# Performance work log

Measured on AMD Instinct MI355X. Metric: run time of the kernel, lower is better.

The kernel has to match this reference:

```python
import jax, jax.numpy as jnp
import numpy as np

NUM_CODES = 1024
CODE_DIM = 64
EMA_DECAY = 0.99
COMMIT_W = 0.25
EPS = 1e-5
B = 262144


def setup_inputs() -> dict:
    key = jax.random.key(0)
    k1, k2, k3, k4 = jax.random.split(key, 4)
    z = jax.random.normal(k1, (B, CODE_DIM), dtype=jnp.float32)
    weight = jax.random.normal(k2, (NUM_CODES, CODE_DIM), dtype=jnp.float32)
    ema_cluster_size = jax.random.uniform(k3, (NUM_CODES,), dtype=jnp.float32)
    ema_embed_sum = jax.random.normal(k4, (NUM_CODES, CODE_DIM), dtype=jnp.float32)
    return {"z": z, "weight": weight, "ema_cluster_size": ema_cluster_size,
            "ema_embed_sum": ema_embed_sum}


def reference(z, weight, ema_cluster_size, ema_embed_sum):
    # Squared Euclidean distances (argmin equivalent to cdist argmin)
    # d2[b,k] = ||z_b||^2 - 2 z_b . w_k + ||w_k||^2
    z2 = jnp.sum(z * z, axis=-1, keepdims=True)          # (B, 1)
    w2 = jnp.sum(weight * weight, axis=-1)               # (K,)
    d2 = z2 - 2.0 * (z @ weight.T) + w2[None, :]         # (B, K)
    indices = jnp.argmin(d2, axis=-1)                    # (B,)
    z_q = weight[indices]                                # gather with OLD weights

    # EMA codebook update (training, ema_update=True)
    ones = jnp.ones((z.shape[0],), dtype=z.dtype)
    cluster_size = jax.ops.segment_sum(ones, indices, num_segments=NUM_CODES)
    embed_sum = jax.ops.segment_sum(z, indices, num_segments=NUM_CODES)
    new_cs = EMA_DECAY * ema_cluster_size + (1.0 - EMA_DECAY) * cluster_size
    new_es = EMA_DECAY * ema_embed_sum + (1.0 - EMA_DECAY) * embed_sum
    n = jnp.sum(new_cs)
    smoothed = (new_cs + EPS) / (n + NUM_CODES * EPS) * n
    new_weight = new_es / smoothed[:, None]

    # commitment loss (z detached in torch; pure value here)
    vq_loss = COMMIT_W * jnp.mean((z - z_q) ** 2)

    # straight-through estimator
    z_q_st = z + jax.lax.stop_gradient(z_q - z)
    return z_q_st, indices, vq_loss, new_cs, new_es, new_weight
```

## Files before the change

### kernel.cpp

```cpp
#include <hip/hip_runtime.h>

typedef __attribute__((ext_vector_type(8))) short bf16x8;
typedef __attribute__((ext_vector_type(4))) float f32x4;

#define B_ROWS 262144
#define K_CODES 1024
#define DIM 64
#define SDELTA 0.015f

#define OUT_ZQ 0
#define OUT_IDX 16777216
#define OUT_LOSS 17039360
#define OUT_NEWCS 17039361
#define OUT_NEWES 17040385
#define OUT_NEWW 17105921

#define WS_LOSS   0
#define WS_QCOUNT 1
#define WS_W2     16
#define WS_SMOOTH 1040
#define WS_WHIP   2064
#define WS_WLOP   34832
#define WS_CPART  67600
#define WS_EPART  100368
#define WS_MINI   2197520
#define WS_QUEUE  2459664

static __device__ __forceinline__ unsigned short f2bf(float x) {
    unsigned u = __float_as_uint(x);
    return (unsigned short)((u + 0x7fffu + ((u >> 16) & 1u)) >> 16);
}
static __device__ __forceinline__ float bf2f(unsigned short u) {
    return __uint_as_float(((unsigned)u) << 16);
}

static __device__ __forceinline__ float red16(float x) {
    int v;
    v = __builtin_amdgcn_update_dpp(0, __float_as_int(x), 0x128, 0xF, 0xF, true);
    x += __int_as_float(v);
    v = __builtin_amdgcn_update_dpp(0, __float_as_int(x), 0x124, 0xF, 0xF, true);
    x += __int_as_float(v);
    v = __builtin_amdgcn_update_dpp(0, __float_as_int(x), 0x122, 0xF, 0xF, true);
    x += __int_as_float(v);
    v = __builtin_amdgcn_update_dpp(0, __float_as_int(x), 0x121, 0xF, 0xF, true);
    x += __int_as_float(v);
    return x;
}

static __device__ __forceinline__ void cvt_frag(const float* zrow, bf16x8& hi, bf16x8& lo) {
    float4 f0 = *(const float4*)zrow;
    float4 f1 = *(const float4*)(zrow + 4);
    float tf[8] = {f0.x, f0.y, f0.z, f0.w, f1.x, f1.y, f1.z, f1.w};
#pragma unroll
    for (int j = 0; j < 8; ++j) {
        unsigned short h = f2bf(tf[j]);
        hi[j] = (short)h;
        lo[j] = (short)f2bf(tf[j] - bf2f(h));
    }
}

__global__ __launch_bounds__(256) void vq_prep(const float* __restrict__ w,
                                               float* __restrict__ ws) {
    int b = blockIdx.x, tid = threadIdx.x;
    if (b < 4) {
        int k = b * 256 + tid;
        const float4* w4 = (const float4*)(w + (size_t)k * DIM);
        float s = 0.f;
#pragma unroll
        for (int j = 0; j < 16; ++j) {
            float4 v = w4[j];
            s += v.x * v.x + v.y * v.y + v.z * v.z + v.w * v.w;
        }
        ws[WS_W2 + k] = s;
    } else {
        int i = (b - 4) * 256 + tid;
        int p = i & 1023, c = i >> 10;
        int code = c * 128 + ((p >> 7) << 4) + (p & 15);
        int octet = ((p >> 6) & 1) * 4 + ((p >> 4) & 3);
        const float* src = w + (size_t)code * DIM + octet * 8;
        float4 f0 = *(const float4*)src;
        float4 f1 = *(const float4*)(src + 4);
        float tf[8] = {f0.x, f0.y, f0.z, f0.w, f1.x, f1.y, f1.z, f1.w};
        bf16x8 hv, lv;
#pragma unroll
        for (int j = 0; j < 8; ++j) {
            unsigned short hb = f2bf(tf[j]);
            hv[j] = (short)hb;
            lv[j] = (short)f2bf(tf[j] - bf2f(hb));
        }
        ((bf16x8*)(ws + WS_WHIP))[i] = hv;
        ((bf16x8*)(ws + WS_WLOP))[i] = lv;
    }
}

__global__ __launch_bounds__(256)
__attribute__((amdgpu_waves_per_eu(3, 4))) void vq_screen_kernel(
    const float* __restrict__ z, float* __restrict__ ws) {
    __shared__ float lds_w2h[K_CODES];

    int tid = threadIdx.x;
    int l = tid & 63, wave = tid >> 6;
    int m = l & 15, q = l >> 4;

    {
        float4 wv = ((const float4*)(ws + WS_W2))[tid];
        float4 hv;
        hv.x = -0.5f * wv.x;
        hv.y = -0.5f * wv.y;
        hv.z = -0.5f * wv.z;
        hv.w = -0.5f * wv.w;
        *(float4*)&lds_w2h[tid * 4] = hv;
    }

    int rowbase = blockIdx.x * 256 + wave * 64;
    bf16x8 zhi[4][2], zlo[4][2];
#pragma unroll
    for (int g = 0; g < 4; ++g) {
        const float* zr = z + (size_t)(rowbase + g * 16 + m) * DIM + q * 8;
        cvt_frag(zr, zhi[g][0], zlo[g][0]);
        cvt_frag(zr + 32, zhi[g][1], zlo[g][1]);
    }

    float kv[4], k2[4];
#pragma unroll
    for (int g = 0; g < 4; ++g) { kv[g] = -3.4e38f; k2[g] = -3.4e38f; }

    const bf16x8* __restrict__ gh = (const bf16x8*)(ws + WS_WHIP);
    const bf16x8* __restrict__ gl = (const bf16x8*)(ws + WS_WLOP);

    __syncthreads();

    for (int cch = 0; cch < 8; ++cch) {
#pragma unroll 2
        for (int tg = 0; tg < 8; ++tg) {
            int gi = cch * 1024 + tg * 128 + l;
            bf16x8 bh0 = gh[gi];
            bf16x8 bh1 = gh[gi + 64];
            bf16x8 bl0 = gl[gi];
            bf16x8 bl1 = gl[gi + 64];
            unsigned cbase = (unsigned)(cch * 128 + tg * 16 + q * 4);
            unsigned ibase = (unsigned)((cch * 8 + tg) * 4);
            f32x4 cinit = *(const f32x4*)&lds_w2h[cbase];
#pragma unroll
            for (int g = 0; g < 4; ++g) {
                f32x4 acc = cinit;
                acc = __builtin_amdgcn_mfma_f32_16x16x32_bf16(bh0, zlo[g][0], acc, 0, 0, 0);
                acc = __builtin_amdgcn_mfma_f32_16x16x32_bf16(bl0, zhi[g][0], acc, 0, 0, 0);
                acc = __builtin_amdgcn_mfma_f32_16x16x32_bf16(bh1, zlo[g][1], acc, 0, 0, 0);
                acc = __builtin_amdgcn_mfma_f32_16x16x32_bf16(bl1, zhi[g][1], acc, 0, 0, 0);
                acc = __builtin_amdgcn_mfma_f32_16x16x32_bf16(bh0, zhi[g][0], acc, 0, 0, 0);
                acc = __builtin_amdgcn_mfma_f32_16x16x32_bf16(bh1, zhi[g][1], acc, 0, 0, 0);
                float a0 = __uint_as_float((__float_as_uint(acc[0]) & 0xFFFFFF00u) | ibase);
                float a1 = __uint_as_float((__float_as_uint(acc[1]) & 0xFFFFFF00u) | (ibase + 1u));
                float a2 = __uint_as_float((__float_as_uint(acc[2]) & 0xFFFFFF00u) | (ibase + 2u));
                float a3 = __uint_as_float((__float_as_uint(acc[3]) & 0xFFFFFF00u) | (ibase + 3u));
                float m01 = fmaxf(a0, a1), n01 = fminf(a0, a1);
                float m23 = fmaxf(a2, a3), n23 = fminf(a2, a3);
                float top = fmaxf(m01, m23);
                float sec = fmaxf(fmaxf(fminf(m01, m23), n01), n23);
                k2[g] = fmaxf(fmaxf(k2[g], sec), fminf(kv[g], top));
                kv[g] = fmaxf(kv[g], top);
            }
        }
    }

    float mv[4], m2[4];
    int mi[4];
#pragma unroll
    for (int g = 0; g < 4; ++g) {
        unsigned kb = __float_as_uint(kv[g]);
        unsigned i8 = kb & 255u;
        mi[g] = (int)((i8 >> 5) * 128 + ((i8 >> 2) & 7) * 16 + (unsigned)q * 4 + (i8 & 3));
        mv[g] = __uint_as_float(kb & 0xFFFFFF00u);
        m2[g] = __uint_as_float(__float_as_uint(k2[g]) & 0xFFFFFF00u);
    }
#pragma unroll
    for (int o = 16; o < 64; o <<= 1) {
#pragma unroll
        for (int g = 0; g < 4; ++g) {
            float ov = __shfl_xor(mv[g], o, 64);
            float ov2 = __shfl_xor(m2[g], o, 64);
            int oi = __shfl_xor(mi[g], o, 64);
            float nm2 = fmaxf(fmaxf(m2[g], ov2), fminf(mv[g], ov));
            bool take = (ov > mv[g]) || (ov == mv[g] && oi < mi[g]);
            mv[g] = take ? ov : mv[g];
            mi[g] = take ? oi : mi[g];
            m2[g] = nm2;
        }
    }
    if (q == 0) {
#pragma unroll
        for (int g = 0; g < 4; ++g) {
            bool amb = (mv[g] - m2[g]) <= SDELTA;
            ((int*)ws)[WS_MINI + rowbase + g * 16 + m] = mi[g] | (amb ? 0x80000000 : 0);
        }
    }
}

__global__ __launch_bounds__(256) void vq_gather_kernel(
    const float* __restrict__ z, const float* __restrict__ w,
    float* __restrict__ ws, float* __restrict__ out) {
    __shared__ float lred[4];
    int tid = threadIdx.x;
    int lane = tid & 63, wave = tid >> 6;
    int rsub = lane >> 4;
    int d4 = lane & 15;
    int wavebase = blockIdx.x * 256 + wave * 64;

    int encv[16];
#pragma unroll
    for (int s = 0; s < 16; ++s)
        encv[s] = ((const int*)ws)[WS_MINI + wavebase + s * 4 + rsub];

    float lsum = 0.f;
#pragma unroll
    for (int s = 0; s < 16; ++s) {
        int row = wavebase + s * 4 + rsub;
        int enc = encv[s];
        if (enc >= 0) {
            float4 x = ((const float4*)(z + (size_t)row * DIM))[d4];
            float4 qv = ((const float4*)(w + (size_t)enc * DIM))[d4];
            float4 st;
            st.x = x.x + (qv.x - x.x);
            st.y = x.y + (qv.y - x.y);
            st.z = x.z + (qv.z - x.z);
            st.w = x.w + (qv.w - x.w);
            ((float4*)(out + OUT_ZQ + (size_t)row * DIM))[d4] = st;
            float e0 = x.x - qv.x, e1 = x.y - qv.y, e2 = x.z - qv.z, e3 = x.w - qv.w;
            lsum += e0 * e0;
            lsum += e1 * e1;
            lsum += e2 * e2;
            lsum += e3 * e3;
            if (d4 == 0) out[OUT_IDX + row] = (float)enc;
        } else if (d4 == 0) {
            int pos = atomicAdd((int*)ws + WS_QCOUNT, 1);
            ((int*)ws)[WS_QUEUE + pos] = row;
        }
    }
#pragma unroll
    for (int o = 32; o; o >>= 1) lsum += __shfl_down(lsum, o, 64);
    if (lane == 0) lred[wave] = lsum;
    __syncthreads();
    if (tid == 0) atomicAdd(ws + WS_LOSS, lred[0] + lred[1] + lred[2] + lred[3]);
}

__global__ __launch_bounds__(256) void vq_fixup_kernel(
    const float* __restrict__ z, const float* __restrict__ w,
    float* __restrict__ ws, float* __restrict__ out) {
    const float* __restrict__ w2 = ws + WS_W2;
    __shared__ float sdd[4][4];
    __shared__ int sbi[4][4];
    int count = ((const int*)ws)[WS_QCOUNT];
    int tid = threadIdx.x;
    int lane = tid & 63, wave = tid >> 6;
    int sub = lane >> 4, d4 = lane & 15;
    float lacc = 0.f;
    for (int q0 = blockIdx.x * 4; q0 < count; q0 += gridDim.x * 4) {
        int qi = q0 + sub;
        bool active = qi < count;
        int row = ((const int*)ws)[WS_QUEUE + (active ? qi : 0)];
        float4 zx = ((const float4*)(z + (size_t)row * DIM))[d4];
        float zp = zx.x * zx.x;
        zp = fmaf(zx.y, zx.y, zp);
        zp = fmaf(zx.z, zx.z, zp);
        zp = fmaf(zx.w, zx.w, zp);
        float z2 = red16(zp);
        float best = 3.4e38f;
        int bi = 0;
        int c0 = wave * 256;
#pragma unroll 4
        for (int cc = 0; cc < 256; ++cc) {
            int c = c0 + cc;
            float4 wv4 = ((const float4*)(w + (size_t)c * DIM))[d4];
            float p = zx.x * wv4.x;
            p = fmaf(zx.y, wv4.y, p);
            p = fmaf(zx.z, wv4.z, p);
            p = fmaf(zx.w, wv4.w, p);
            p = red16(p);
            float dd = (z2 - 2.f * p) + w2[c];
            if (dd < best) { best = dd; bi = c; }
        }
        if (d4 == 0) { sdd[wave][sub] = best; sbi[wave][sub] = bi; }
        __syncthreads();
        if (wave == 0 && active) {
            float fb = sdd[0][sub];
            int fbi = sbi[0][sub];
#pragma unroll
            for (int v = 1; v < 4; ++v) {
                float od = sdd[v][sub];
                int oi = sbi[v][sub];
                if (od < fb || (od == fb && oi < fbi)) { fb = od; fbi = oi; }
            }
            float4 qv = ((const float4*)(w + (size_t)fbi * DIM))[d4];
            float4 st;
            st.x = zx.x + (qv.x - zx.x);
            st.y = zx.y + (qv.y - zx.y);
            st.z = zx.z + (qv.z - zx.z);
            st.w = zx.w + (qv.w - zx.w);
            ((float4*)(out + OUT_ZQ + (size_t)row * DIM))[d4] = st;
            float e0 = zx.x - qv.x, e1 = zx.y - qv.y;
            float e2 = zx.z - qv.z, e3 = zx.w - qv.w;
            float ls = e0 * e0 + e1 * e1 + e2 * e2 + e3 * e3;
            ls = red16(ls);
            if (d4 == 0) {
                out[OUT_IDX + row] = (float)fbi;
                lacc += ls;
            }
        }
        __syncthreads();
    }
    lacc += __shfl_xor(lacc, 16, 64);
    lacc += __shfl_xor(lacc, 32, 64);
    if (tid == 0 && lacc != 0.f) atomicAdd(ws + WS_LOSS, lacc);
}

__global__ __launch_bounds__(1024) void vq_embed_kernel(
    const float* __restrict__ z, const float* __restrict__ idx_f,
    float* __restrict__ ws) {
    __shared__ float eacc[128 * DIM];
    __shared__ float ecnt[128];
    __shared__ int lists[16][256];
    int b = blockIdx.x;
    int cs = b & 7, rs = b >> 3;
    float lo = (float)(cs * 128), hi = lo + 128.f;
    int tid = threadIdx.x;
    int wave = tid >> 6, lane = tid & 63;

#pragma unroll
    for (int j = 0; j < 8; ++j) eacc[j * 1024 + tid] = 0.f;
    if (tid < 128) ecnt[tid] = 0.f;
    __syncthreads();

    const float4* idx4 = (const float4*)idx_f;
    unsigned long long lanebits = (1ull << lane) - 1ull;
    for (int it = 0; it < 2; ++it) {
        int base = rs * 8192 + wave * 512 + it * 256;
        float4 f = idx4[(base >> 2) + lane];
        int cnt = 0;
#pragma unroll
        for (int c = 0; c < 4; ++c) {
            float fv = (c == 0) ? f.x : (c == 1) ? f.y : (c == 2) ? f.z : f.w;
            bool match = (fv >= lo && fv < hi);
            unsigned long long mmask = __ballot(match);
            if (match) {
                int pos = cnt + __popcll(mmask & lanebits);
                int row = base + 4 * lane + c;
                int local = (int)fv - cs * 128;
                lists[wave][pos] = (row << 7) | local;
                atomicAdd(&ecnt[local], 1.f);
            }
            cnt += __popcll(mmask);
        }
        int j = 0;
        for (; j + 4 <= cnt; j += 4) {
            int e0 = lists[wave][j], e1 = lists[wave][j + 1];
            int e2 = lists[wave][j + 2], e3 = lists[wave][j + 3];
            float v0 = z[(size_t)(e0 >> 7) * DIM + lane];
            float v1 = z[(size_t)(e1 >> 7) * DIM + lane];
            float v2 = z[(size_t)(e2 >> 7) * DIM + lane];
            float v3 = z[(size_t)(e3 >> 7) * DIM + lane];
            atomicAdd(&eacc[(e0 & 127) * DIM + lane], v0);
            atomicAdd(&eacc[(e1 & 127) * DIM + lane], v1);
            atomicAdd(&eacc[(e2 & 127) * DIM + lane], v2);
            atomicAdd(&eacc[(e3 & 127) * DIM + lane], v3);
        }
        for (; j < cnt; ++j) {
            int e = lists[wave][j];
            float v = z[(size_t)(e >> 7) * DIM + lane];
            atomicAdd(&eacc[(e & 127) * DIM + lane], v);
        }
    }
    __syncthreads();
#pragma unroll
    for (int j = 0; j < 8; ++j)
        ws[WS_EPART + (size_t)b * 8192 + j * 1024 + tid] = eacc[j * 1024 + tid];
    if (tid < 128) ws[WS_CPART + b * 128 + tid] = ecnt[tid];
}

__global__ __launch_bounds__(1024) void vq_finalize1_kernel(
    const float* __restrict__ ema_cs, float* __restrict__ ws,
    float* __restrict__ out) {
    int k = threadIdx.x;
    int cs = k >> 7, local = k & 127;
    float c = 0.f;
#pragma unroll
    for (int rs = 0; rs < 32; ++rs) c += ws[WS_CPART + (rs * 8 + cs) * 128 + local];
    float nc = 0.99f * ema_cs[k] + 0.01f * c;
    out[OUT_NEWCS + k] = nc;

    float s = nc;
#pragma unroll
    for (int o = 32; o; o >>= 1) s += __shfl_down(s, o, 64);
    __shared__ float red[16];
    __shared__ float n_sh;
    if ((k & 63) == 0) red[k >> 6] = s;
    __syncthreads();
    if (k == 0) {
        float n = 0.f;
#pragma unroll
        for (int i = 0; i < 16; ++i) n += red[i];
        n_sh = n;
        out[OUT_LOSS] = 0.25f * (ws[WS_LOSS] / 16777216.0f);
    }
    __syncthreads();
    float n = n_sh;
    ws[WS_SMOOTH + k] = (nc + 1e-5f) / (n + 0.01024f) * n;
}

__global__ __launch_bounds__(256) void vq_finalize2_kernel(
    const float* __restrict__ ema_es, const float* __restrict__ ws,
    float* __restrict__ out) {
    int i = blockIdx.x * 256 + threadIdx.x;
    int code = i >> 6, dim = i & 63;
    int cs = code >> 7, local = code & 127;
    float e = 0.f;
#pragma unroll
    for (int rs = 0; rs < 32; ++rs)
        e += ws[WS_EPART + (size_t)(rs * 8 + cs) * 8192 + local * DIM + dim];
    float es = 0.99f * ema_es[i] + 0.01f * e;
    out[OUT_NEWES + i] = es;
    out[OUT_NEWW + i] = es / ws[WS_SMOOTH + code];
}

extern "C" void kernel_launch(void* const* d_in, const int* in_sizes, int n_in,
                              void* d_out, int out_size, void* d_ws, size_t ws_size,
                              hipStream_t stream) {
    const float* z = (const float*)d_in[0];
    const float* weight = (const float*)d_in[1];
    const float* ema_cs = (const float*)d_in[2];
    const float* ema_es = (const float*)d_in[3];
    float* out = (float*)d_out;
    float* ws = (float*)d_ws;

    hipMemsetAsync(ws, 0, 64, stream);
    vq_prep<<<36, 256, 0, stream>>>(weight, ws);
    vq_screen_kernel<<<B_ROWS / 256, 256, 0, stream>>>(z, ws);
    vq_gather_kernel<<<B_ROWS / 256, 256, 0, stream>>>(z, weight, ws, out);
    vq_fixup_kernel<<<512, 256, 0, stream>>>(z, weight, ws, out);
    vq_embed_kernel<<<256, 1024, 0, stream>>>(z, out + OUT_IDX, ws);
    vq_finalize1_kernel<<<1, 1024, 0, stream>>>(ema_cs, ws, out);
    vq_finalize2_kernel<<<256, 256, 0, stream>>>(ema_es, ws, out);
}
```

Before: 390.7 us.

## Fuse gather/straight-through output into screen kernel, dropping the index round-trip

The separate gather kernel is removed and its work is folded into the tail of the screening kernel. Each row's z values are rebuilt from the bf16 hi/lo split already held in registers, and the winning codeword is read directly. The kernel then writes z_q_st, the index and the loss partial, and queues ambiguous rows for fixup. This removes one launch, the write and reread of the per-row index buffer, and the second read of z from global memory. In exchange the screen kernel gains register pressure and divergent global stores. The output is z_hi+z_lo rather than the original fp32 z, which may differ slightly in the last bits.

```diff
diff --git a/kernel.cpp b/kernel.cpp
--- a/kernel.cpp
+++ b/kernel.cpp
@@ -23,7 +23,6 @@
 #define WS_WLOP   34832
 #define WS_CPART  67600
 #define WS_EPART  100368
-#define WS_MINI   2197520
 #define WS_QUEUE  2459664
 
 static __device__ __forceinline__ unsigned short f2bf(float x) {
@@ -95,8 +94,10 @@
 
 __global__ __launch_bounds__(256)
 __attribute__((amdgpu_waves_per_eu(3, 4))) void vq_screen_kernel(
-    const float* __restrict__ z, float* __restrict__ ws) {
+    const float* __restrict__ z, const float* __restrict__ w,
+    float* __restrict__ ws, float* __restrict__ out) {
     __shared__ float lds_w2h[K_CODES];
+    __shared__ float lred[4];
 
     int tid = threadIdx.x;
     int l = tid & 63, wave = tid >> 6;
@@ -188,58 +189,50 @@
             m2[g] = nm2;
         }
     }
-    if (q == 0) {
-#pragma unroll
-        for (int g = 0; g < 4; ++g) {
-            bool amb = (mv[g] - m2[g]) <= SDELTA;
-            ((int*)ws)[WS_MINI + rowbase + g * 16 + m] = mi[g] | (amb ? 0x80000000 : 0);
-        }
-    }
-}
-
-__global__ __launch_bounds__(256) void vq_gather_kernel(
-    const float* __restrict__ z, const float* __restrict__ w,
-    float* __restrict__ ws, float* __restrict__ out) {
-    __shared__ float lred[4];
-    int tid = threadIdx.x;
-    int lane = tid & 63, wave = tid >> 6;
-    int rsub = lane >> 4;
-    int d4 = lane & 15;
-    int wavebase = blockIdx.x * 256 + wave * 64;
-
-    int encv[16];
-#pragma unroll
-    for (int s = 0; s < 16; ++s)
-        encv[s] = ((const int*)ws)[WS_MINI + wavebase + s * 4 + rsub];
 
     float lsum = 0.f;
 #pragma unroll
-    for (int s = 0; s < 16; ++s) {
-        int row = wavebase + s * 4 + rsub;
-        int enc = encv[s];
-        if (enc >= 0) {
-            float4 x = ((const float4*)(z + (size_t)row * DIM))[d4];
-            float4 qv = ((const float4*)(w + (size_t)enc * DIM))[d4];
-            float4 st;
-            st.x = x.x + (qv.x - x.x);
-            st.y = x.y + (qv.y - x.y);
-            st.z = x.z + (qv.z - x.z);
-            st.w = x.w + (qv.w - x.w);
-            ((float4*)(out + OUT_ZQ + (size_t)row * DIM))[d4] = st;
-            float e0 = x.x - qv.x, e1 = x.y - qv.y, e2 = x.z - qv.z, e3 = x.w - qv.w;
-            lsum += e0 * e0;
-            lsum += e1 * e1;
-            lsum += e2 * e2;
-            lsum += e3 * e3;
-            if (d4 == 0) out[OUT_IDX + row] = (float)enc;
-        } else if (d4 == 0) {
-            int pos = atomicAdd((int*)ws + WS_QCOUNT, 1);
-            ((int*)ws)[WS_QUEUE + pos] = row;
+    for (int g = 0; g < 4; ++g) {
+        int row = rowbase + g * 16 + m;
+        bool amb = (mv[g] - m2[g]) <= SDELTA;
+        if (amb) {
+            if (q == 0) {
+                int pos = atomicAdd((int*)ws + WS_QCOUNT, 1);
+                ((int*)ws)[WS_QUEUE + pos] = row;
+            }
+        } else {
+            int enc = mi[g];
+            const float* wr = w + (size_t)enc * DIM + q * 8;
+            float4 qa = *(const float4*)wr;
+            float4 qb = *(const float4*)(wr + 4);
+            float4 qc = *(const float4*)(wr + 32);
+            float4 qd = *(const float4*)(wr + 36);
+            float qv[16] = {qa.x, qa.y, qa.z, qa.w, qb.x, qb.y, qb.z, qb.w,
+                            qc.x, qc.y, qc.z, qc.w, qd.x, qd.y, qd.z, qd.w};
+            float st[16];
+#pragma unroll
+            for (int j = 0; j < 8; ++j) {
+                float x0 = bf2f((unsigned short)zhi[g][0][j]) +
+                           bf2f((unsigned short)zlo[g][0][j]);
+                float x1 = bf2f((unsigned short)zhi[g][1][j]) +
+                           bf2f((unsigned short)zlo[g][1][j]);
+                st[j] = x0 + (qv[j] - x0);
+                st[8 + j] = x1 + (qv[8 + j] - x1);
+                float e0 = x0 - qv[j], e1 = x1 - qv[8 + j];
+                lsum += e0 * e0;
+                lsum += e1 * e1;
+            }
+            float* op = out + OUT_ZQ + (size_t)row * DIM + q * 8;
+            *(float4*)op = make_float4(st[0], st[1], st[2], st[3]);
+            *(float4*)(op + 4) = make_float4(st[4], st[5], st[6], st[7]);
+            *(float4*)(op + 32) = make_float4(st[8], st[9], st[10], st[11]);
+            *(float4*)(op + 36) = make_float4(st[12], st[13], st[14], st[15]);
+            if (q == 0) out[OUT_IDX + row] = (float)enc;
         }
     }
 #pragma unroll
     for (int o = 32; o; o >>= 1) lsum += __shfl_down(lsum, o, 64);
-    if (lane == 0) lred[wave] = lsum;
+    if (l == 0) lred[wave] = lsum;
     __syncthreads();
     if (tid == 0) atomicAdd(ws + WS_LOSS, lred[0] + lred[1] + lred[2] + lred[3]);
 }
@@ -434,8 +427,7 @@
 
     hipMemsetAsync(ws, 0, 64, stream);
     vq_prep<<<36, 256, 0, stream>>>(weight, ws);
-    vq_screen_kernel<<<B_ROWS / 256, 256, 0, stream>>>(z, ws);
-    vq_gather_kernel<<<B_ROWS / 256, 256, 0, stream>>>(z, weight, ws, out);
+    vq_screen_kernel<<<B_ROWS / 256, 256, 0, stream>>>(z, weight, ws, out);
     vq_fixup_kernel<<<512, 256, 0, stream>>>(z, weight, ws, out);
     vq_embed_kernel<<<256, 1024, 0, stream>>>(z, out + OUT_IDX, ws);
     vq_finalize1_kernel<<<1, 1024, 0, stream>>>(ema_cs, ws, out);
```

New measurement: 409.9 us. +4.9%, slower.
